# Optimization experiments

Hardware: AMD Instinct MI355X
Metric: run time of the kernel (lower is better)

The kernel has to match this reference:

```python
import jax, jax.numpy as jnp
import numpy as np

N_NODES = 100000
N_EDGES = 3200000
D_IN = 256
D_HID = 32
N_CLS = 40
K_HOPS = 3


def setup_inputs() -> dict:
    key = jax.random.key(0)
    ks = jax.random.split(key, 6)
    x = jax.random.normal(ks[0], (N_NODES, D_IN), dtype=jnp.float32)
    edge_index = jax.random.randint(ks[1], (2, N_EDGES), 0, N_NODES, dtype=jnp.int64)
    edge_attr = jax.random.uniform(ks[2], (N_EDGES, 1), dtype=jnp.float32)
    W_conv = jax.random.normal(ks[3], (D_HID, D_IN), dtype=jnp.float32) / np.sqrt(D_IN)
    b_conv = jnp.zeros((D_HID,), dtype=jnp.float32)
    W_fc = jax.random.normal(ks[4], (N_CLS, D_HID), dtype=jnp.float32) * np.sqrt(2.0 / D_HID)
    b_fc = jnp.zeros((N_CLS,), dtype=jnp.float32)
    return {"x": x, "edge_index": edge_index, "edge_attr": edge_attr,
            "W_conv": W_conv, "b_conv": b_conv, "W_fc": W_fc, "b_fc": b_fc}


def _gcn_norm(edge_index, edge_weight, num_nodes):
    # add self-loops with weight 1 (PyG gcn_norm default)
    loop = jnp.arange(num_nodes, dtype=edge_index.dtype)
    row = jnp.concatenate([edge_index[0], loop])
    col = jnp.concatenate([edge_index[1], loop])
    w = jnp.concatenate([edge_weight, jnp.ones((num_nodes,), edge_weight.dtype)])
    deg = jax.ops.segment_sum(w, col, num_segments=num_nodes)
    deg_inv_sqrt = jnp.where(deg > 0, jax.lax.rsqrt(deg), 0.0)
    norm = deg_inv_sqrt[row] * w * deg_inv_sqrt[col]
    return row, col, norm


def reference(x, edge_index, edge_attr, W_conv, b_conv, W_fc, b_fc):
    N = x.shape[0]
    row, col, norm = _gcn_norm(edge_index, edge_attr.squeeze(-1), N)
    # K-hop symmetric-normalized diffusion: x <- (D^-1/2 (A+I) D^-1/2) x
    h = x
    for _ in range(K_HOPS):
        h = jax.ops.segment_sum(norm[:, None] * h[row], col, num_segments=N)
    h = h @ W_conv.T + b_conv          # SGConv linear
    h = jax.nn.elu(h)
    h = h @ W_fc.T + b_fc              # classifier
    return jax.nn.log_softmax(h, axis=1)
```

## Files before the change

kernel.cpp:

```cpp
#include <hip/hip_runtime.h>
#include <math.h>

#define N_NODES 100000
#define N_EDGES 3200000
#define D_IN    256
#define D_HID   32
#define N_CLS   40

#define NCOARSE 3125
#define NB_A    256
#define CHUNK_A 12500
#define NB_C    256
#define CHUNK_C 12500

typedef unsigned int u32;
typedef unsigned short u16;
typedef unsigned long long u64;

__device__ __forceinline__ float bf2f(u16 v) {
    return __uint_as_float(((u32)v) << 16);
}
__device__ __forceinline__ u16 f2bf(float f) {
    u32 u = __float_as_uint(f);
    u32 r = u + 0x7FFFu + ((u >> 16) & 1u);
    return (u16)(r >> 16);
}


__global__ __launch_bounds__(256) void k_hist(const int* __restrict__ col,
                                              int* __restrict__ chist) {
    __shared__ u32 h[NCOARSE];
    for (int j = threadIdx.x; j < NCOARSE; j += 256) h[j] = 0;
    __syncthreads();
    int s = blockIdx.x * CHUNK_A;
    for (int i = s + threadIdx.x; i < s + CHUNK_A; i += 256)
        atomicAdd(&h[((u32)col[i]) >> 5], 1u);
    __syncthreads();
    for (int j = threadIdx.x; j < NCOARSE; j += 256) {
        u32 c = h[j];
        if (c) atomicAdd((u32*)&chist[j], c);
    }
}


__global__ __launch_bounds__(1024) void k_scanc(const int* __restrict__ chist,
                                                int* __restrict__ cstart,
                                                int* __restrict__ ccur) {
    __shared__ int ts[1024];
    int t = threadIdx.x;
    int idx = t * 4;
    int v0 = (idx     < NCOARSE) ? chist[idx]     : 0;
    int v1 = (idx + 1 < NCOARSE) ? chist[idx + 1] : 0;
    int v2 = (idx + 2 < NCOARSE) ? chist[idx + 2] : 0;
    int v3 = (idx + 3 < NCOARSE) ? chist[idx + 3] : 0;
    int s = v0 + v1 + v2 + v3;
    ts[t] = s;
    __syncthreads();
    for (int off = 1; off < 1024; off <<= 1) {
        int u = (t >= off) ? ts[t - off] : 0;
        __syncthreads();
        ts[t] += u;
        __syncthreads();
    }
    int run = ts[t] - s;
    if (idx < NCOARSE)     { cstart[idx]     = run; ccur[idx]     = run; run += v0; }
    if (idx + 1 < NCOARSE) { cstart[idx + 1] = run; ccur[idx + 1] = run; run += v1; }
    if (idx + 2 < NCOARSE) { cstart[idx + 2] = run; ccur[idx + 2] = run; run += v2; }
    if (idx + 3 < NCOARSE) { cstart[idx + 3] = run; ccur[idx + 3] = run; run += v3; }
    if (t == 1023) cstart[NCOARSE] = ts[t];
}


__global__ __launch_bounds__(256) void k_coarse(const int* __restrict__ row,
                                                const int* __restrict__ col,
                                                const float* __restrict__ w,
                                                int* __restrict__ ccur,
                                                uint2* __restrict__ coarse) {
    __shared__ u32 lcnt[NCOARSE];
    __shared__ u32 lbase[NCOARSE];
    for (int j = threadIdx.x; j < NCOARSE; j += 256) lcnt[j] = 0;
    __syncthreads();
    int s = blockIdx.x * CHUNK_C;
    for (int i = s + threadIdx.x; i < s + CHUNK_C; i += 256)
        atomicAdd(&lcnt[((u32)col[i]) >> 5], 1u);
    __syncthreads();
    for (int j = threadIdx.x; j < NCOARSE; j += 256) {
        u32 c = lcnt[j];
        lbase[j] = c ? atomicAdd((u32*)&ccur[j], c) : 0u;
    }
    __syncthreads();
    for (int i = s + threadIdx.x; i < s + CHUNK_C; i += 256) {
        u32 c = (u32)col[i];
        u32 b = c >> 5;
        u32 pos = atomicAdd(&lbase[b], 1u);
        u32 key = ((c & 31u) << 17) | (u32)row[i];
        coarse[pos] = make_uint2(key, __float_as_uint(w[i]));
    }
}


__global__ __launch_bounds__(256) void k_deg(const uint2* __restrict__ coarse,
                                             const int* __restrict__ cstart,
                                             float* __restrict__ dis,
                                             int* __restrict__ startp) {
    __shared__ u32 c32[32];
    __shared__ float ws32[32];
    int b = blockIdx.x;
    int s = cstart[b], e = cstart[b + 1];
    if (threadIdx.x < 32) { c32[threadIdx.x] = 0; ws32[threadIdx.x] = 0.f; }
    __syncthreads();
    for (int i = s + threadIdx.x; i < e; i += 256) {
        uint2 p = coarse[i];
        u32 f = (p.x >> 17) & 31u;
        atomicAdd(&c32[f], 1u);
        atomicAdd(&ws32[f], __uint_as_float(p.y));
    }
    __syncthreads();
    if (threadIdx.x < 32) {
        int node = b * 32 + threadIdx.x;
        dis[node] = rsqrtf(1.0f + ws32[threadIdx.x]);
    }
    if (threadIdx.x == 0) {
        int run = s;
        for (int f = 0; f < 32; ++f) { startp[b * 32 + f] = run; run += (int)c32[f]; }
        if (b == NCOARSE - 1) startp[N_NODES] = run;
    }
}


__global__ __launch_bounds__(256) void k_fine(const uint2* __restrict__ coarse,
                                              const int* __restrict__ cstart,
                                              const int* __restrict__ startp,
                                              const float* __restrict__ dis,
                                              u32* __restrict__ csr) {
    __shared__ u32 cur[32];
    int b = blockIdx.x;
    int s = cstart[b], e = cstart[b + 1];
    if (threadIdx.x < 32) cur[threadIdx.x] = (u32)startp[b * 32 + threadIdx.x];
    __syncthreads();
    for (int i = s + threadIdx.x; i < e; i += 256) {
        uint2 p = coarse[i];
        u32 f = (p.x >> 17) & 31u;
        u32 r = p.x & 0x1FFFFu;
        float m = dis[r] * __uint_as_float(p.y);
        u32 q = (u32)(m * 32768.0f + 0.5f);
        if (q > 32767u) q = 32767u;
        u32 pos = atomicAdd(&cur[f], 1u);
        csr[pos] = (r << 15) | q;
    }
}


#define LSTRIDE 260

__global__ __launch_bounds__(256) void k_gemm1(const float* __restrict__ x,
                                               const float* __restrict__ Wc,
                                               u16* __restrict__ g) {
    __shared__ float xs[32 * LSTRIDE];
    __shared__ float wsl[32 * LSTRIDE];
    const int tid  = threadIdx.x;
    const int base = blockIdx.x * 32;

    for (int i = tid; i < 2048; i += 256) {
        int r = i >> 6, j = i & 63;
        float4 v = reinterpret_cast<const float4*>(x)[(size_t)(base + r) * 64 + j];
        *reinterpret_cast<float4*>(&xs[r * LSTRIDE + j * 4]) = v;
    }
    for (int i = tid; i < 2048; i += 256) {
        int r = i >> 6, j = i & 63;
        float4 v = reinterpret_cast<const float4*>(Wc)[i];
        *reinterpret_cast<float4*>(&wsl[r * LSTRIDE + j * 4]) = v;
    }
    __syncthreads();

    const int node = tid >> 3;
    const int og   = tid & 7;
    float4 acc = make_float4(0.f, 0.f, 0.f, 0.f);
    const float* xrow = &xs[node * LSTRIDE];
    const float* w0 = &wsl[(og     ) * LSTRIDE];
    const float* w1 = &wsl[(og +  8) * LSTRIDE];
    const float* w2 = &wsl[(og + 16) * LSTRIDE];
    const float* w3 = &wsl[(og + 24) * LSTRIDE];

#pragma unroll 4
    for (int k = 0; k < 256; k += 4) {
        float4 xv = *reinterpret_cast<const float4*>(&xrow[k]);
        float4 a4 = *reinterpret_cast<const float4*>(&w0[k]);
        float4 b4 = *reinterpret_cast<const float4*>(&w1[k]);
        float4 c4 = *reinterpret_cast<const float4*>(&w2[k]);
        float4 d4 = *reinterpret_cast<const float4*>(&w3[k]);
        acc.x += xv.x * a4.x + xv.y * a4.y + xv.z * a4.z + xv.w * a4.w;
        acc.y += xv.x * b4.x + xv.y * b4.y + xv.z * b4.z + xv.w * b4.w;
        acc.z += xv.x * c4.x + xv.y * c4.y + xv.z * c4.z + xv.w * c4.w;
        acc.w += xv.x * d4.x + xv.y * d4.y + xv.z * d4.z + xv.w * d4.w;
    }
    size_t gb = (size_t)(base + node) * D_HID;
    g[gb + og     ] = f2bf(acc.x);
    g[gb + og +  8] = f2bf(acc.y);
    g[gb + og + 16] = f2bf(acc.z);
    g[gb + og + 24] = f2bf(acc.w);
}


__global__ __launch_bounds__(256) void k_pull(const int* __restrict__ start,
                                              const u32* __restrict__ csr,
                                              const float* __restrict__ dis,
                                              const u16* __restrict__ h,
                                              u16* __restrict__ out) {
    int g    = blockIdx.x * 8 + (threadIdx.x >> 5);
    int lane = threadIdx.x & 31;
    if (g >= N_NODES) return;

    int s = start[g];
    int e = start[g + 1];
    float ds  = dis[g];
    float acc = ds * bf2f(h[(size_t)g * D_HID + lane]);

    for (int base = s; base < e; base += 32) {
        int idx = base + lane;
        u32 p = (idx < e) ? csr[idx] : 0u;
        int rem = e - base;
        for (int jj = 0; jj < 32; jj += 8) {
            if (jj >= rem) break;
#pragma unroll
            for (int j = 0; j < 8; ++j) {
                u32 pj = __shfl(p, jj + j, 32);
                float nv = (float)(pj & 32767u) * (1.0f / 32768.0f);
                u32 src = pj >> 15;
                acc += nv * bf2f(h[(size_t)src * D_HID + lane]);
            }
        }
    }
    out[(size_t)g * D_HID + lane] = f2bf(ds * acc);
}


__global__ __launch_bounds__(256) void k_final(const u16* __restrict__ h,
                                               const float* __restrict__ bc,
                                               const float* __restrict__ Wfc,
                                               const float* __restrict__ bf,
                                               float* __restrict__ out) {
    __shared__ float wf[N_CLS * D_HID];
    __shared__ float bcs[D_HID];
    __shared__ float bfs[N_CLS];
    const int tid = threadIdx.x;
    for (int i = tid; i < N_CLS * D_HID; i += 256) wf[i] = Wfc[i];
    if (tid < D_HID) bcs[tid] = bc[tid];
    if (tid < N_CLS) bfs[tid] = bf[tid];
    __syncthreads();

    int node = blockIdx.x * 256 + tid;
    if (node >= N_NODES) return;

    float a[D_HID];
    const u32* hp = reinterpret_cast<const u32*>(h + (size_t)node * D_HID);
#pragma unroll
    for (int j = 0; j < 16; ++j) {
        u32 v = hp[j];
        float z0 = bf2f((u16)(v & 0xFFFFu)) + bcs[j * 2 + 0];
        float z1 = bf2f((u16)(v >> 16))     + bcs[j * 2 + 1];
        a[j * 2 + 0] = z0 > 0.f ? z0 : expm1f(z0);
        a[j * 2 + 1] = z1 > 0.f ? z1 : expm1f(z1);
    }

    float logits[N_CLS];
    float m = -1e30f;
#pragma unroll
    for (int c = 0; c < N_CLS; ++c) {
        float accv = bfs[c];
        const float* wr = &wf[c * D_HID];
#pragma unroll
        for (int o = 0; o < D_HID; ++o) accv += a[o] * wr[o];
        logits[c] = accv;
        m = fmaxf(m, accv);
    }
    float sum = 0.f;
#pragma unroll
    for (int c = 0; c < N_CLS; ++c) sum += expf(logits[c] - m);
    float lse = m + logf(sum);
    float* op = out + (size_t)node * N_CLS;
#pragma unroll
    for (int c = 0; c < N_CLS; ++c) op[c] = logits[c] - lse;
}


extern "C" void kernel_launch(void* const* d_in, const int* in_sizes, int n_in,
                              void* d_out, int out_size, void* d_ws, size_t ws_size,
                              hipStream_t stream) {
    const float* x   = (const float*)d_in[0];
    const int*   ei  = (const int*)d_in[1];
    const float* ea  = (const float*)d_in[2];
    const float* Wc  = (const float*)d_in[3];
    const float* bc  = (const float*)d_in[4];
    const float* Wfc = (const float*)d_in[5];
    const float* bf  = (const float*)d_in[6];
    float* out = (float*)d_out;
    float* ws  = (float*)d_ws;

    const int* row = ei;
    const int* col = ei + N_EDGES;

    float* dis    = ws;
    int*   chist  = (int*)(ws + 100000);
    int*   ccur   = (int*)(ws + 103128);
    int*   cstart = (int*)(ws + 106256);
    int*   startp = (int*)(ws + 109384);
    uint2* coarse = (uint2*)(ws + 209388);
    u32*   csr    = (u32*)(ws + 6609388);
    u16*   bufA   = (u16*)(ws + 9809388);
    u16*   bufB   = (u16*)(ws + 11409388);

    const int GN = (N_NODES + 255) / 256;
    const int GP = (N_NODES + 7) / 8;

    hipMemsetAsync(chist, 0, NCOARSE * sizeof(int), stream);
    k_hist  <<<NB_A, 256, 0, stream>>>(col, chist);
    k_scanc <<<1, 1024, 0, stream>>>(chist, cstart, ccur);
    k_coarse<<<NB_C, 256, 0, stream>>>(row, col, ea, ccur, coarse);
    k_deg   <<<NCOARSE, 256, 0, stream>>>(coarse, cstart, dis, startp);
    k_fine  <<<NCOARSE, 256, 0, stream>>>(coarse, cstart, startp, dis, csr);

    k_gemm1 <<<N_NODES / 32, 256, 0, stream>>>(x, Wc, bufA);

    k_pull  <<<GP, 256, 0, stream>>>(startp, csr, dis, bufA, bufB);
    k_pull  <<<GP, 256, 0, stream>>>(startp, csr, dis, bufB, bufA);
    k_pull  <<<GP, 256, 0, stream>>>(startp, csr, dis, bufA, bufB);

    k_final <<<GN, 256, 0, stream>>>(bufB, bc, Wfc, bf, out);
}
```

Before: 563.0 us.

## Rebuild CSR via 512-node partitions with staged scatter and fold norm into pull

Replaces the 3125-bucket coarse sort and separate degree/fine kernels with a 196-partition counting sort. It uses a per-block histogram matrix, so there are no global atomics, and scatters through a shared-memory staging buffer so writes land in runs. A single per-partition kernel then computes degrees and the local prefix scan and builds the CSR. Edge weights no longer depend on dis, so the D^-1/2 scaling moves into the GEMM output and the pull epilogue (dis squared on the intermediate hops). This removes kernel launches, the atomic contention on the global cursor and the dependent dis gather per edge. The cost is heavier per-partition blocks with fewer of them, and bufA/bufB now alias the coarse buffer region.

```diff
diff --git a/kernel.cpp b/kernel.cpp
--- a/kernel.cpp
+++ b/kernel.cpp
@@ -7,15 +7,14 @@
 #define D_HID   32
 #define N_CLS   40
 
-#define NCOARSE 3125
-#define NB_A    256
-#define CHUNK_A 12500
-#define NB_C    256
-#define CHUNK_C 12500
+#define NPART  196
+#define HROW   200
+#define NB1    256
+#define CHUNK1 12500
+#define SUB    2500
 
 typedef unsigned int u32;
 typedef unsigned short u16;
-typedef unsigned long long u64;
 
 __device__ __forceinline__ float bf2f(u16 v) {
     return __uint_as_float(((u32)v) << 16);
@@ -27,126 +26,145 @@
 }
 
 
-__global__ __launch_bounds__(256) void k_hist(const int* __restrict__ col,
-                                              int* __restrict__ chist) {
-    __shared__ u32 h[NCOARSE];
-    for (int j = threadIdx.x; j < NCOARSE; j += 256) h[j] = 0;
-    __syncthreads();
-    int s = blockIdx.x * CHUNK_A;
-    for (int i = s + threadIdx.x; i < s + CHUNK_A; i += 256)
-        atomicAdd(&h[((u32)col[i]) >> 5], 1u);
-    __syncthreads();
-    for (int j = threadIdx.x; j < NCOARSE; j += 256) {
-        u32 c = h[j];
-        if (c) atomicAdd((u32*)&chist[j], c);
-    }
-}
-
-
-__global__ __launch_bounds__(1024) void k_scanc(const int* __restrict__ chist,
-                                                int* __restrict__ cstart,
-                                                int* __restrict__ ccur) {
-    __shared__ int ts[1024];
+__global__ __launch_bounds__(256) void k_histA(const int* __restrict__ col,
+                                               u32* __restrict__ histmat) {
+    __shared__ u32 h[256];
     int t = threadIdx.x;
-    int idx = t * 4;
-    int v0 = (idx     < NCOARSE) ? chist[idx]     : 0;
-    int v1 = (idx + 1 < NCOARSE) ? chist[idx + 1] : 0;
-    int v2 = (idx + 2 < NCOARSE) ? chist[idx + 2] : 0;
-    int v3 = (idx + 3 < NCOARSE) ? chist[idx + 3] : 0;
-    int s = v0 + v1 + v2 + v3;
-    ts[t] = s;
-    __syncthreads();
-    for (int off = 1; off < 1024; off <<= 1) {
-        int u = (t >= off) ? ts[t - off] : 0;
-        __syncthreads();
-        ts[t] += u;
-        __syncthreads();
-    }
-    int run = ts[t] - s;
-    if (idx < NCOARSE)     { cstart[idx]     = run; ccur[idx]     = run; run += v0; }
-    if (idx + 1 < NCOARSE) { cstart[idx + 1] = run; ccur[idx + 1] = run; run += v1; }
-    if (idx + 2 < NCOARSE) { cstart[idx + 2] = run; ccur[idx + 2] = run; run += v2; }
-    if (idx + 3 < NCOARSE) { cstart[idx + 3] = run; ccur[idx + 3] = run; run += v3; }
-    if (t == 1023) cstart[NCOARSE] = ts[t];
-}
-
-
-__global__ __launch_bounds__(256) void k_coarse(const int* __restrict__ row,
-                                                const int* __restrict__ col,
-                                                const float* __restrict__ w,
-                                                int* __restrict__ ccur,
-                                                uint2* __restrict__ coarse) {
-    __shared__ u32 lcnt[NCOARSE];
-    __shared__ u32 lbase[NCOARSE];
-    for (int j = threadIdx.x; j < NCOARSE; j += 256) lcnt[j] = 0;
-    __syncthreads();
-    int s = blockIdx.x * CHUNK_C;
-    for (int i = s + threadIdx.x; i < s + CHUNK_C; i += 256)
-        atomicAdd(&lcnt[((u32)col[i]) >> 5], 1u);
-    __syncthreads();
-    for (int j = threadIdx.x; j < NCOARSE; j += 256) {
-        u32 c = lcnt[j];
-        lbase[j] = c ? atomicAdd((u32*)&ccur[j], c) : 0u;
-    }
-    __syncthreads();
-    for (int i = s + threadIdx.x; i < s + CHUNK_C; i += 256) {
-        u32 c = (u32)col[i];
-        u32 b = c >> 5;
-        u32 pos = atomicAdd(&lbase[b], 1u);
-        u32 key = ((c & 31u) << 17) | (u32)row[i];
-        coarse[pos] = make_uint2(key, __float_as_uint(w[i]));
-    }
-}
-
-
-__global__ __launch_bounds__(256) void k_deg(const uint2* __restrict__ coarse,
-                                             const int* __restrict__ cstart,
-                                             float* __restrict__ dis,
-                                             int* __restrict__ startp) {
-    __shared__ u32 c32[32];
-    __shared__ float ws32[32];
-    int b = blockIdx.x;
-    int s = cstart[b], e = cstart[b + 1];
-    if (threadIdx.x < 32) { c32[threadIdx.x] = 0; ws32[threadIdx.x] = 0.f; }
-    __syncthreads();
-    for (int i = s + threadIdx.x; i < e; i += 256) {
-        uint2 p = coarse[i];
-        u32 f = (p.x >> 17) & 31u;
-        atomicAdd(&c32[f], 1u);
-        atomicAdd(&ws32[f], __uint_as_float(p.y));
-    }
-    __syncthreads();
-    if (threadIdx.x < 32) {
-        int node = b * 32 + threadIdx.x;
-        dis[node] = rsqrtf(1.0f + ws32[threadIdx.x]);
-    }
-    if (threadIdx.x == 0) {
-        int run = s;
-        for (int f = 0; f < 32; ++f) { startp[b * 32 + f] = run; run += (int)c32[f]; }
-        if (b == NCOARSE - 1) startp[N_NODES] = run;
-    }
-}
-
-
-__global__ __launch_bounds__(256) void k_fine(const uint2* __restrict__ coarse,
+    h[t] = 0;
+    __syncthreads();
+    int s = blockIdx.x * CHUNK1;
+    for (int i = s + t; i < s + CHUNK1; i += 256)
+        atomicAdd(&h[((u32)col[i]) >> 9], 1u);
+    __syncthreads();
+    if (t < HROW) histmat[blockIdx.x * HROW + t] = (t < NPART) ? h[t] : 0u;
+}
+
+
+__global__ __launch_bounds__(256) void k_scanA(u32* __restrict__ histmat,
+                                               int* __restrict__ cstart) {
+    __shared__ u32 sc[256];
+    int p = threadIdx.x;
+    u32 run = 0;
+    for (int b = 0; b < NB1; ++b) {
+        u32 v = (p < NPART) ? histmat[b * HROW + p] : 0u;
+        if (p < NPART) histmat[b * HROW + p] = run;
+        run += v;
+    }
+    u32 own = (p < NPART) ? run : 0u;
+    sc[p] = own;
+    __syncthreads();
+    for (int off = 1; off < 256; off <<= 1) {
+        u32 v = (p >= off) ? sc[p - off] : 0u;
+        __syncthreads();
+        sc[p] += v;
+        __syncthreads();
+    }
+    if (p < NPART) cstart[p] = (int)(sc[p] - own);
+    if (p == NPART - 1) cstart[NPART] = (int)sc[p];
+}
+
+
+__global__ __launch_bounds__(256) void k_part(const int* __restrict__ row,
+                                              const int* __restrict__ col,
+                                              const float* __restrict__ w,
+                                              const u32* __restrict__ histmat,
                                               const int* __restrict__ cstart,
-                                              const int* __restrict__ startp,
-                                              const float* __restrict__ dis,
-                                              u32* __restrict__ csr) {
-    __shared__ u32 cur[32];
-    int b = blockIdx.x;
-    int s = cstart[b], e = cstart[b + 1];
-    if (threadIdx.x < 32) cur[threadIdx.x] = (u32)startp[b * 32 + threadIdx.x];
-    __syncthreads();
-    for (int i = s + threadIdx.x; i < e; i += 256) {
-        uint2 p = coarse[i];
-        u32 f = (p.x >> 17) & 31u;
-        u32 r = p.x & 0x1FFFFu;
-        float m = dis[r] * __uint_as_float(p.y);
-        u32 q = (u32)(m * 32768.0f + 0.5f);
+                                              uint2* __restrict__ coarse) {
+    __shared__ u32 shist[256], sscan[256], scur[256], gbase[256], rcur[256];
+    __shared__ uint2 stage[SUB];
+    __shared__ u32 gdst[SUB];
+    int t = threadIdx.x;
+    rcur[t] = (t < NPART) ? ((u32)cstart[t] + histmat[blockIdx.x * HROW + t]) : 0u;
+    int s0 = blockIdx.x * CHUNK1;
+
+    for (int sc_ = 0; sc_ < CHUNK1; sc_ += SUB) {
+        int s = s0 + sc_;
+        shist[t] = 0;
+        __syncthreads();
+        for (int i = s + t; i < s + SUB; i += 256)
+            atomicAdd(&shist[((u32)col[i]) >> 9], 1u);
+        __syncthreads();
+        u32 own = shist[t];
+        sscan[t] = own;
+        __syncthreads();
+        for (int off = 1; off < 256; off <<= 1) {
+            u32 v = (t >= off) ? sscan[t - off] : 0u;
+            __syncthreads();
+            sscan[t] += v;
+            __syncthreads();
+        }
+        u32 exc = sscan[t] - own;
+        scur[t]  = exc;
+        gbase[t] = rcur[t] - exc;
+        __syncthreads();
+        for (int i = s + t; i < s + SUB; i += 256) {
+            u32 c = (u32)col[i];
+            u32 pid = c >> 9;
+            u32 pos = atomicAdd(&scur[pid], 1u);
+            stage[pos] = make_uint2(((c & 511u) << 17) | (u32)row[i], __float_as_uint(w[i]));
+            gdst[pos]  = gbase[pid] + pos;
+        }
+        __syncthreads();
+        for (int i = t; i < SUB; i += 256) coarse[gdst[i]] = stage[i];
+        rcur[t] += shist[t];
+        __syncthreads();
+    }
+}
+
+
+__global__ __launch_bounds__(256) void k_part2(const uint2* __restrict__ coarse,
+                                               const int* __restrict__ cstart,
+                                               float* __restrict__ dis,
+                                               int* __restrict__ startp,
+                                               u32* __restrict__ csr) {
+    __shared__ float wsuml[512];
+    __shared__ u32 cntl[512];
+    __shared__ u32 curl[512];
+    __shared__ u32 psum[256];
+    int p = blockIdx.x, t = threadIdx.x;
+    int s = cstart[p], e = cstart[p + 1];
+    int nbase = p << 9;
+
+    cntl[t] = 0; cntl[t + 256] = 0;
+    wsuml[t] = 0.f; wsuml[t + 256] = 0.f;
+    __syncthreads();
+    for (int i = s + t; i < e; i += 256) {
+        uint2 en = coarse[i];
+        u32 l = en.x >> 17;
+        atomicAdd(&cntl[l], 1u);
+        atomicAdd(&wsuml[l], __uint_as_float(en.y));
+    }
+    __syncthreads();
+    for (int l = t; l < 512; l += 256) {
+        int node = nbase + l;
+        if (node < N_NODES) dis[node] = rsqrtf(1.0f + wsuml[l]);
+    }
+    u32 a0 = cntl[2 * t], a1 = cntl[2 * t + 1];
+    psum[t] = a0 + a1;
+    __syncthreads();
+    for (int off = 1; off < 256; off <<= 1) {
+        u32 v = (t >= off) ? psum[t - off] : 0u;
+        __syncthreads();
+        psum[t] += v;
+        __syncthreads();
+    }
+    u32 excl = psum[t] - (a0 + a1);
+    u32 c0 = (u32)s + excl, c1 = c0 + a0;
+    curl[2 * t] = c0; curl[2 * t + 1] = c1;
+    int n0 = nbase + 2 * t, n1 = n0 + 1;
+    if (n0 < N_NODES) startp[n0] = (int)c0;
+    if (n1 < N_NODES) startp[n1] = (int)c1;
+    if (p == NPART - 1 && t == 255) startp[N_NODES] = e;
+    __syncthreads();
+    for (int i = s + t; i < e; i += 256) {
+        uint2 en = coarse[i];
+        u32 l = en.x >> 17;
+        u32 src = en.x & 0x1FFFFu;
+        float wv = __uint_as_float(en.y);
+        u32 q = (u32)(wv * 32768.0f + 0.5f);
         if (q > 32767u) q = 32767u;
-        u32 pos = atomicAdd(&cur[f], 1u);
-        csr[pos] = (r << 15) | q;
+        u32 pos = atomicAdd(&curl[l], 1u);
+        csr[pos] = (src << 15) | q;
     }
 }
 
@@ -155,6 +173,7 @@
 
 __global__ __launch_bounds__(256) void k_gemm1(const float* __restrict__ x,
                                                const float* __restrict__ Wc,
+                                               const float* __restrict__ dis,
                                                u16* __restrict__ g) {
     __shared__ float xs[32 * LSTRIDE];
     __shared__ float wsl[32 * LSTRIDE];
@@ -194,11 +213,12 @@
         acc.z += xv.x * c4.x + xv.y * c4.y + xv.z * c4.z + xv.w * c4.w;
         acc.w += xv.x * d4.x + xv.y * d4.y + xv.z * d4.z + xv.w * d4.w;
     }
+    float dv = dis[base + node];
     size_t gb = (size_t)(base + node) * D_HID;
-    g[gb + og     ] = f2bf(acc.x);
-    g[gb + og +  8] = f2bf(acc.y);
-    g[gb + og + 16] = f2bf(acc.z);
-    g[gb + og + 24] = f2bf(acc.w);
+    g[gb + og     ] = f2bf(acc.x * dv);
+    g[gb + og +  8] = f2bf(acc.y * dv);
+    g[gb + og + 16] = f2bf(acc.z * dv);
+    g[gb + og + 24] = f2bf(acc.w * dv);
 }
 
 
@@ -206,15 +226,15 @@
                                               const u32* __restrict__ csr,
                                               const float* __restrict__ dis,
                                               const u16* __restrict__ h,
-                                              u16* __restrict__ out) {
+                                              u16* __restrict__ out,
+                                              int sq) {
     int g    = blockIdx.x * 8 + (threadIdx.x >> 5);
     int lane = threadIdx.x & 31;
     if (g >= N_NODES) return;
 
     int s = start[g];
     int e = start[g + 1];
-    float ds  = dis[g];
-    float acc = ds * bf2f(h[(size_t)g * D_HID + lane]);
+    float acc = bf2f(h[(size_t)g * D_HID + lane]);
 
     for (int base = s; base < e; base += 32) {
         int idx = base + lane;
@@ -231,7 +251,9 @@
             }
         }
     }
-    out[(size_t)g * D_HID + lane] = f2bf(ds * acc);
+    float sc = dis[g];
+    if (sq) sc *= sc;
+    out[(size_t)g * D_HID + lane] = f2bf(sc * acc);
 }
 
 
@@ -300,31 +322,28 @@
     const int* row = ei;
     const int* col = ei + N_EDGES;
 
-    float* dis    = ws;
-    int*   chist  = (int*)(ws + 100000);
-    int*   ccur   = (int*)(ws + 103128);
-    int*   cstart = (int*)(ws + 106256);
-    int*   startp = (int*)(ws + 109384);
-    uint2* coarse = (uint2*)(ws + 209388);
-    u32*   csr    = (u32*)(ws + 6609388);
-    u16*   bufA   = (u16*)(ws + 9809388);
-    u16*   bufB   = (u16*)(ws + 11409388);
+    float* dis     = ws;
+    int*   cstart  = (int*)(ws + 100000);
+    u32*   histmat = (u32*)(ws + 100224);
+    int*   startp  = (int*)(ws + 151424);
+    uint2* coarse  = (uint2*)(ws + 251428);
+    u32*   csr     = (u32*)(ws + 6651428);
+    u16*   bufA    = (u16*)(ws + 251428);
+    u16*   bufB    = (u16*)(ws + 1851428);
 
     const int GN = (N_NODES + 255) / 256;
     const int GP = (N_NODES + 7) / 8;
 
-    hipMemsetAsync(chist, 0, NCOARSE * sizeof(int), stream);
-    k_hist  <<<NB_A, 256, 0, stream>>>(col, chist);
-    k_scanc <<<1, 1024, 0, stream>>>(chist, cstart, ccur);
-    k_coarse<<<NB_C, 256, 0, stream>>>(row, col, ea, ccur, coarse);
-    k_deg   <<<NCOARSE, 256, 0, stream>>>(coarse, cstart, dis, startp);
-    k_fine  <<<NCOARSE, 256, 0, stream>>>(coarse, cstart, startp, dis, csr);
-
-    k_gemm1 <<<N_NODES / 32, 256, 0, stream>>>(x, Wc, bufA);
-
-    k_pull  <<<GP, 256, 0, stream>>>(startp, csr, dis, bufA, bufB);
-    k_pull  <<<GP, 256, 0, stream>>>(startp, csr, dis, bufB, bufA);
-    k_pull  <<<GP, 256, 0, stream>>>(startp, csr, dis, bufA, bufB);
+    k_histA <<<NB1, 256, 0, stream>>>(col, histmat);
+    k_scanA <<<1, 256, 0, stream>>>(histmat, cstart);
+    k_part  <<<NB1, 256, 0, stream>>>(row, col, ea, histmat, cstart, coarse);
+    k_part2 <<<NPART, 256, 0, stream>>>(coarse, cstart, dis, startp, csr);
+
+    k_gemm1 <<<N_NODES / 32, 256, 0, stream>>>(x, Wc, dis, bufA);
+
+    k_pull  <<<GP, 256, 0, stream>>>(startp, csr, dis, bufA, bufB, 1);
+    k_pull  <<<GP, 256, 0, stream>>>(startp, csr, dis, bufB, bufA, 1);
+    k_pull  <<<GP, 256, 0, stream>>>(startp, csr, dis, bufA, bufB, 0);
 
     k_final <<<GN, 256, 0, stream>>>(bufB, bc, Wfc, bf, out);
 }
```

Result: no change. 565.0 us (+0.4%).
